# Performance work log

Hardware: AMD Instinct MI355X
Metric: run time of the kernel (lower is better)

## Reference

```python
import jax, jax.numpy as jnp
import numpy as np

SEQ, BATCH, IN = 512, 64, 1024
H, L = 512, 2


def setup_inputs() -> dict:
    key = jax.random.key(0)
    ks = jax.random.split(key, 5)
    s = 0.02
    return {
        "x": jax.random.normal(ks[0], (SEQ, BATCH, IN), dtype=jnp.float32),
        "W_ih": jax.random.normal(ks[1], (L, 2, 4 * H, IN), dtype=jnp.float32) * s,
        "b_ih": jax.random.normal(ks[2], (L, 2, 4 * H), dtype=jnp.float32) * s,
        "W_hh": jax.random.normal(ks[3], (L, 2, 4 * H, H), dtype=jnp.float32) * s,
        "b_hh": jax.random.normal(ks[4], (L, 2, 4 * H), dtype=jnp.float32) * s,
    }


def _run_direction(xs, Wi, bi, Wh, bh, hidden):
    # Precompute the input projection for all timesteps in one big GEMM.
    pre = jnp.einsum("tbd,gd->tbg", xs, Wi) + bi  # [T, B, 4H]

    def step(carry, p):
        h, c = carry
        gates = p + h @ Wh.T + bh
        i, f, g, o = jnp.split(gates, 4, axis=-1)
        # NOTE: faithful to the source module's (nonstandard) gating:
        #   c_t = c_{t-1} * sigmoid(i) + sigmoid(f) * tanh(g)
        c = c * jax.nn.sigmoid(i) + jax.nn.sigmoid(f) * jnp.tanh(g)
        h = jnp.tanh(c) * jax.nn.sigmoid(o)
        return (h, c), h

    B = xs.shape[1]
    h0 = jnp.zeros((B, hidden), xs.dtype)
    c0 = jnp.zeros((B, hidden), xs.dtype)
    _, hs = jax.lax.scan(step, (h0, c0), pre)
    return hs  # [T, B, H]


def reference(x, W_ih, b_ih, W_hh, b_hh):
    hidden = W_hh.shape[-1]
    num_layers = W_ih.shape[0]
    inp = x  # [T, B, D]
    for l in range(num_layers):
        fwd = _run_direction(inp, W_ih[l, 0], b_ih[l, 0], W_hh[l, 0], b_hh[l, 0], hidden)
        bwd = _run_direction(inp[::-1], W_ih[l, 1], b_ih[l, 1], W_hh[l, 1], b_hh[l, 1], hidden)[::-1]
        inp = jnp.concatenate([fwd, bwd], axis=-1)  # [T, B, 2H]
    return inp
```

## Files before the change

kernel.cpp:

```cpp
#include <hip/hip_runtime.h>

#define TSEQ 512
#define BATCH 64
#define DIN 1024
#define HID 512
#define G4 2048
#define CHK 64

typedef __attribute__((ext_vector_type(8))) short short8;
typedef __attribute__((ext_vector_type(4))) float floatx4;

__device__ __forceinline__ floatx4 mfma16(short8 a, short8 b, floatx4 c) {
  return __builtin_amdgcn_mfma_f32_16x16x32_bf16(a, b, c, 0, 0, 0);
}

__device__ __forceinline__ unsigned short f2bf(float f) {
  unsigned int u = __float_as_uint(f);
  unsigned int r = (u + 0x7fffu + ((u >> 16) & 1u)) >> 16;
  return (unsigned short)r;
}

__device__ __forceinline__ float sigm(float x) { return 1.f / (1.f + __expf(-x)); }
__device__ __forceinline__ float tanh_f(float x) {
  float xx = fminf(fmaxf(x, -15.f), 15.f);
  float e = __expf(2.f * xx);
  return (e - 1.f) / (e + 1.f);
}

__global__ void k_convert_x(const float* __restrict__ x, unsigned short* __restrict__ xbf, int n4) {
  int i = blockIdx.x * 256 + threadIdx.x;
  if (i >= n4) return;
  floatx4 v = reinterpret_cast<const floatx4*>(x)[i];
  union { unsigned short us[4]; unsigned long long ull; } pk;
  pk.us[0] = f2bf(v[0]); pk.us[1] = f2bf(v[1]); pk.us[2] = f2bf(v[2]); pk.us[3] = f2bf(v[3]);
  reinterpret_cast<unsigned long long*>(xbf)[i] = pk.ull;
}

__global__ void k_prep_w(const float* __restrict__ W, unsigned short* __restrict__ Wf, int K) {
  int mt = blockIdx.x, kt = blockIdx.y, ld = blockIdx.z;
  int lane = threadIdx.x;
  int rp = mt * 16 + (lane & 15);
  int row = (rp & 3) * HID + (rp >> 2);
  int k0 = kt * 32 + (lane >> 4) * 8;
  const float* src = W + (size_t)ld * G4 * K + (size_t)row * K + k0;
  unsigned short* dst = Wf + (size_t)ld * G4 * K + (((size_t)mt * (K / 32) + kt) * 64 + lane) * 8;
  for (int j = 0; j < 8; ++j) dst[j] = f2bf(src[j]);
}

__global__ void k_prep_bias(const float* __restrict__ bih, const float* __restrict__ bhh,
                            float* __restrict__ biasf) {
  int i = blockIdx.x * 256 + threadIdx.x;
  int ld = i >> 11;
  int rp = i & 2047;
  int row = (rp & 3) * HID + (rp >> 2);
  biasf[i] = bih[ld * G4 + row] + bhh[ld * G4 + row];
}

__global__ __launch_bounds__(256, 2) void k_proj(
    const unsigned short* __restrict__ xin,
    const unsigned short* __restrict__ Wf,
    const float* __restrict__ biasf,
    float* __restrict__ pre,
    int t0) {
  const int dir = blockIdx.z;
  const int w = threadIdx.x >> 6;
  const int lane = threadIdx.x & 63;
  const int quad = lane >> 4, col = lane & 15;
  const int tloc = blockIdx.y * 4 + w;
  const int tg = dir ? (TSEQ - 1 - (t0 + tloc)) : (t0 + tloc);
  const unsigned short* Wd = Wf + (size_t)dir * G4 * DIN;
  const unsigned short* xrow = xin + (size_t)tg * BATCH * DIN;

  floatx4 acc[8][4];
#pragma unroll
  for (int mi = 0; mi < 8; ++mi)
#pragma unroll
    for (int ni = 0; ni < 4; ++ni) acc[mi][ni] = (floatx4){0.f, 0.f, 0.f, 0.f};

#pragma unroll 4
  for (int kt = 0; kt < 32; ++kt) {
    short8 bfr[4];
#pragma unroll
    for (int ni = 0; ni < 4; ++ni) {
      int b = ni * 16 + col;
      bfr[ni] = *reinterpret_cast<const short8*>(xrow + (size_t)b * DIN + kt * 32 + quad * 8);
    }
#pragma unroll
    for (int mi = 0; mi < 8; ++mi) {
      size_t mt = (size_t)(blockIdx.x * 8 + mi);
      short8 afr = *reinterpret_cast<const short8*>(Wd + ((mt * 32 + kt) * 64 + lane) * 8);
#pragma unroll
      for (int ni = 0; ni < 4; ++ni) acc[mi][ni] = mfma16(afr, bfr[ni], acc[mi][ni]);
    }
  }

#pragma unroll
  for (int mi = 0; mi < 8; ++mi) {
    int gbase = blockIdx.x * 128 + mi * 16 + quad * 4;
#pragma unroll
    for (int r = 0; r < 4; ++r) {
      float bv = biasf[dir * G4 + gbase + r];
      float* prow = pre + (((size_t)dir * CHK + tloc) * G4 + gbase + r) * BATCH;
#pragma unroll
      for (int ni = 0; ni < 4; ++ni) prow[ni * 16 + col] = acc[mi][ni][r] + bv;
    }
  }
}

__global__ __launch_bounds__(256, 4) void k_step(
    const unsigned short* __restrict__ Whhf,
    const float* __restrict__ pre,
    unsigned short* act1bf,
    unsigned short* hT2,
    float* cst,
    float* __restrict__ dout,
    int s, int jloc, int layer) {
  const int dir = blockIdx.y;
  const int gb = blockIdx.x;
  const int w = threadIdx.x >> 6;
  const int lane = threadIdx.x & 63;
  const int quad = lane >> 4, col = lane & 15;
  const int b = w * 16 + col;
  const int t = dir ? (TSEQ - 1 - s) : s;

  floatx4 acc[2];
#pragma unroll
  for (int mi = 0; mi < 2; ++mi) {
#pragma unroll
    for (int r = 0; r < 4; ++r) {
      int gp = gb * 32 + mi * 16 + quad * 4 + r;
      acc[mi][r] = pre[(((size_t)dir * CHK + jloc) * G4 + gp) * BATCH + b];
    }
  }

  if (s > 0) {
    const unsigned short* hprev;
    int hstride;
    if (layer == 0) {
      int tp = dir ? t + 1 : t - 1;
      hprev = act1bf + (size_t)tp * BATCH * DIN + dir * HID;
      hstride = DIN;
    } else {
      hprev = hT2 + (size_t)(((s - 1) & 1) * 2 + dir) * BATCH * HID;
      hstride = HID;
    }
    const unsigned short* Wd = Whhf + (size_t)dir * G4 * HID;
#pragma unroll
    for (int kt = 0; kt < 16; ++kt) {
      short8 bfr = *reinterpret_cast<const short8*>(hprev + (size_t)b * hstride + kt * 32 + quad * 8);
#pragma unroll
      for (int mi = 0; mi < 2; ++mi) {
        size_t mt = (size_t)(gb * 2 + mi);
        short8 afr = *reinterpret_cast<const short8*>(Wd + ((mt * 16 + kt) * 64 + lane) * 8);
        acc[mi] = mfma16(afr, bfr, acc[mi]);
      }
    }
  }

  float* cl = cst + ((size_t)layer * 2 + dir) * HID * BATCH;
#pragma unroll
  for (int mi = 0; mi < 2; ++mi) {
    int u = gb * 8 + mi * 4 + quad;
    float si = sigm(acc[mi][0]);
    float sf = sigm(acc[mi][1]);
    float tg = tanh_f(acc[mi][2]);
    float so = sigm(acc[mi][3]);
    float cprev = (s > 0) ? cl[u * BATCH + b] : 0.f;
    float c = cprev * si + sf * tg;
    float h = tanh_f(c) * so;
    cl[u * BATCH + b] = c;
    if (layer == 0) {
      act1bf[((size_t)t * BATCH + b) * DIN + dir * HID + u] = f2bf(h);
    } else {
      hT2[((size_t)((s & 1) * 2 + dir) * BATCH + b) * HID + u] = f2bf(h);
      dout[((size_t)t * BATCH + b) * DIN + dir * HID + u] = h;
    }
  }
}

extern "C" void kernel_launch(void* const* d_in, const int* in_sizes, int n_in,
                              void* d_out, int out_size, void* d_ws, size_t ws_size,
                              hipStream_t stream) {
  const float* x = (const float*)d_in[0];
  const float* W_ih = (const float*)d_in[1];
  const float* b_ih = (const float*)d_in[2];
  const float* W_hh = (const float*)d_in[3];
  const float* b_hh = (const float*)d_in[4];
  float* dout = (float*)d_out;

  char* p = (char*)d_ws;
  auto alloc = [&](size_t bytes) {
    char* r = p;
    p += (bytes + 255) & ~(size_t)255;
    return r;
  };
  unsigned short* xbf    = (unsigned short*)alloc((size_t)TSEQ * BATCH * DIN * 2);
  unsigned short* act1bf = (unsigned short*)alloc((size_t)TSEQ * BATCH * DIN * 2);
  float*          pre    = (float*)alloc((size_t)2 * CHK * G4 * BATCH * 4);
  unsigned short* Wihf   = (unsigned short*)alloc((size_t)4 * G4 * DIN * 2);
  unsigned short* Whhf   = (unsigned short*)alloc((size_t)4 * G4 * HID * 2);
  float*          biasf  = (float*)alloc((size_t)4 * G4 * 4);
  float*          cst    = (float*)alloc((size_t)4 * HID * BATCH * 4);
  unsigned short* hT2    = (unsigned short*)alloc((size_t)4 * BATCH * HID * 2);

  size_t required = (size_t)(p - (char*)d_ws);
  if (ws_size < required) return;

  int n4 = TSEQ * BATCH * DIN / 4;
  k_convert_x<<<dim3((n4 + 255) / 256), dim3(256), 0, stream>>>(x, xbf, n4);
  k_prep_w<<<dim3(G4 / 16, DIN / 32, 4), dim3(64), 0, stream>>>(W_ih, Wihf, DIN);
  k_prep_w<<<dim3(G4 / 16, HID / 32, 4), dim3(64), 0, stream>>>(W_hh, Whhf, HID);
  k_prep_bias<<<dim3(32), dim3(256), 0, stream>>>(b_ih, b_hh, biasf);

  for (int l = 0; l < 2; ++l) {
    const unsigned short* xin = l ? act1bf : xbf;
    const unsigned short* Wfl = Wihf + (size_t)l * 2 * G4 * DIN;
    const unsigned short* Whl = Whhf + (size_t)l * 2 * G4 * HID;
    const float* bfl = biasf + (size_t)l * 2 * G4;
    for (int c = 0; c < TSEQ / CHK; ++c) {
      k_proj<<<dim3(G4 / 128, CHK / 4, 2), dim3(256), 0, stream>>>(xin, Wfl, bfl, pre, c * CHK);
      for (int j = 0; j < CHK; ++j) {
        k_step<<<dim3(G4 / 32, 2), dim3(256), 0, stream>>>(Whl, pre, act1bf, hT2, cst, dout,
                                                           c * CHK + j, j, l);
      }
    }
  }
  (void)in_sizes; (void)n_in; (void)out_size;
}
```

Measured before the change: 7.263 ms.

## Replace per-timestep launches with persistent chunk kernel and grid barrier

Instead of launching one step kernel per timestep, a single kernel now runs all 64 steps of a chunk. A per-direction atomic-counter grid barrier separates the steps. The W_hh fragments stay resident in registers across steps, the cell state is kept in registers, and the next step's preactivations are prefetched. This removes launch overhead and repeated weight and state loads, but it depends on all 128 blocks being co-resident (which holds for this grid) and adds spin-barrier latency at every step.

Result: slower. 12.14 ms (+67.1%).

```diff
diff --git a/kernel.cpp b/kernel.cpp
--- a/kernel.cpp
+++ b/kernel.cpp
@@ -54,6 +54,10 @@
   int rp = i & 2047;
   int row = (rp & 3) * HID + (rp >> 2);
   biasf[i] = bih[ld * G4 + row] + bhh[ld * G4 + row];
+}
+
+__global__ void k_zero_bar(unsigned int* bar) {
+  if (threadIdx.x < 2) bar[threadIdx.x * 64] = 0;
 }
 
 __global__ __launch_bounds__(256, 2) void k_proj(
@@ -107,75 +111,135 @@
   }
 }
 
-__global__ __launch_bounds__(256, 4) void k_step(
+__device__ __forceinline__ void dir_barrier(unsigned int* ctr, unsigned int target) {
+  __syncthreads();
+  if (threadIdx.x == 0) {
+    __threadfence();
+    __hip_atomic_fetch_add(ctr, 1u, __ATOMIC_RELAXED, __HIP_MEMORY_SCOPE_AGENT);
+    while (__hip_atomic_load(ctr, __ATOMIC_RELAXED, __HIP_MEMORY_SCOPE_AGENT) < target) {
+      __builtin_amdgcn_s_sleep(1);
+    }
+    __threadfence();
+  }
+  __syncthreads();
+}
+
+__global__ __launch_bounds__(256, 1) void k_steps(
     const unsigned short* __restrict__ Whhf,
     const float* __restrict__ pre,
     unsigned short* act1bf,
     unsigned short* hT2,
     float* cst,
     float* __restrict__ dout,
-    int s, int jloc, int layer) {
+    unsigned int* bar,
+    int t0, int layer, unsigned int bar_base) {
   const int dir = blockIdx.y;
   const int gb = blockIdx.x;
   const int w = threadIdx.x >> 6;
   const int lane = threadIdx.x & 63;
   const int quad = lane >> 4, col = lane & 15;
   const int b = w * 16 + col;
-  const int t = dir ? (TSEQ - 1 - s) : s;
-
-  floatx4 acc[2];
-#pragma unroll
-  for (int mi = 0; mi < 2; ++mi) {
+  unsigned int* ctr = bar + dir * 64;
+
+  const unsigned short* Wd = Whhf + (size_t)dir * G4 * HID;
+  short8 wfr[16][2];
+#pragma unroll
+  for (int kt = 0; kt < 16; ++kt)
+#pragma unroll
+    for (int mi = 0; mi < 2; ++mi) {
+      size_t mt = (size_t)(gb * 2 + mi);
+      wfr[kt][mi] = *reinterpret_cast<const short8*>(Wd + ((mt * 16 + kt) * 64 + lane) * 8);
+    }
+
+  float* cl = cst + ((size_t)layer * 2 + dir) * HID * BATCH;
+  const int u0 = gb * 8 + quad;
+  const int u1 = gb * 8 + 4 + quad;
+  float c0 = 0.f, c1 = 0.f;
+  if (t0 > 0) { c0 = cl[u0 * BATCH + b]; c1 = cl[u1 * BATCH + b]; }
+
+  float pf[2][4];
+#pragma unroll
+  for (int mi = 0; mi < 2; ++mi)
 #pragma unroll
     for (int r = 0; r < 4; ++r) {
       int gp = gb * 32 + mi * 16 + quad * 4 + r;
-      acc[mi][r] = pre[(((size_t)dir * CHK + jloc) * G4 + gp) * BATCH + b];
-    }
-  }
-
-  if (s > 0) {
-    const unsigned short* hprev;
-    int hstride;
+      pf[mi][r] = pre[(((size_t)dir * CHK + 0) * G4 + gp) * BATCH + b];
+    }
+
+  for (int j = 0; j < CHK; ++j) {
+    const int s = t0 + j;
+    const int t = dir ? (TSEQ - 1 - s) : s;
+
+    floatx4 acc[2];
+#pragma unroll
+    for (int mi = 0; mi < 2; ++mi)
+#pragma unroll
+      for (int r = 0; r < 4; ++r) acc[mi][r] = pf[mi][r];
+
+    if (j + 1 < CHK) {
+#pragma unroll
+      for (int mi = 0; mi < 2; ++mi)
+#pragma unroll
+        for (int r = 0; r < 4; ++r) {
+          int gp = gb * 32 + mi * 16 + quad * 4 + r;
+          pf[mi][r] = pre[(((size_t)dir * CHK + (j + 1)) * G4 + gp) * BATCH + b];
+        }
+    }
+
+    if (s > 0) {
+      const unsigned short* hprev;
+      int hstride;
+      if (layer == 0) {
+        int tp = dir ? t + 1 : t - 1;
+        hprev = act1bf + (size_t)tp * BATCH * DIN + dir * HID;
+        hstride = DIN;
+      } else {
+        hprev = hT2 + (size_t)(((s - 1) & 1) * 2 + dir) * BATCH * HID;
+        hstride = HID;
+      }
+      const unsigned short* hrow = hprev + (size_t)b * hstride;
+#pragma unroll
+      for (int kt = 0; kt < 16; ++kt) {
+        short8 bfr = *reinterpret_cast<const short8*>(hrow + kt * 32 + quad * 8);
+        acc[0] = mfma16(wfr[kt][0], bfr, acc[0]);
+        acc[1] = mfma16(wfr[kt][1], bfr, acc[1]);
+      }
+    }
+
+    float si = sigm(acc[0][0]);
+    float sf = sigm(acc[0][1]);
+    float tg = tanh_f(acc[0][2]);
+    float so = sigm(acc[0][3]);
+    c0 = c0 * si + sf * tg;
+    float h0 = tanh_f(c0) * so;
+
+    si = sigm(acc[1][0]);
+    sf = sigm(acc[1][1]);
+    tg = tanh_f(acc[1][2]);
+    so = sigm(acc[1][3]);
+    c1 = c1 * si + sf * tg;
+    float h1 = tanh_f(c1) * so;
+
     if (layer == 0) {
-      int tp = dir ? t + 1 : t - 1;
-      hprev = act1bf + (size_t)tp * BATCH * DIN + dir * HID;
-      hstride = DIN;
+      unsigned short* arow = act1bf + ((size_t)t * BATCH + b) * DIN + dir * HID;
+      arow[u0] = f2bf(h0);
+      arow[u1] = f2bf(h1);
     } else {
-      hprev = hT2 + (size_t)(((s - 1) & 1) * 2 + dir) * BATCH * HID;
-      hstride = HID;
-    }
-    const unsigned short* Wd = Whhf + (size_t)dir * G4 * HID;
-#pragma unroll
-    for (int kt = 0; kt < 16; ++kt) {
-      short8 bfr = *reinterpret_cast<const short8*>(hprev + (size_t)b * hstride + kt * 32 + quad * 8);
-#pragma unroll
-      for (int mi = 0; mi < 2; ++mi) {
-        size_t mt = (size_t)(gb * 2 + mi);
-        short8 afr = *reinterpret_cast<const short8*>(Wd + ((mt * 16 + kt) * 64 + lane) * 8);
-        acc[mi] = mfma16(afr, bfr, acc[mi]);
-      }
-    }
-  }
-
-  float* cl = cst + ((size_t)layer * 2 + dir) * HID * BATCH;
-#pragma unroll
-  for (int mi = 0; mi < 2; ++mi) {
-    int u = gb * 8 + mi * 4 + quad;
-    float si = sigm(acc[mi][0]);
-    float sf = sigm(acc[mi][1]);
-    float tg = tanh_f(acc[mi][2]);
-    float so = sigm(acc[mi][3]);
-    float cprev = (s > 0) ? cl[u * BATCH + b] : 0.f;
-    float c = cprev * si + sf * tg;
-    float h = tanh_f(c) * so;
-    cl[u * BATCH + b] = c;
-    if (layer == 0) {
-      act1bf[((size_t)t * BATCH + b) * DIN + dir * HID + u] = f2bf(h);
-    } else {
-      hT2[((size_t)((s & 1) * 2 + dir) * BATCH + b) * HID + u] = f2bf(h);
-      dout[((size_t)t * BATCH + b) * DIN + dir * HID + u] = h;
-    }
-  }
+      unsigned short* hrow2 = hT2 + ((size_t)((s & 1) * 2 + dir) * BATCH + b) * HID;
+      hrow2[u0] = f2bf(h0);
+      hrow2[u1] = f2bf(h1);
+      float* drow = dout + ((size_t)t * BATCH + b) * DIN + dir * HID;
+      drow[u0] = h0;
+      drow[u1] = h1;
+    }
+
+    if (j + 1 < CHK) {
+      dir_barrier(ctr, bar_base + (unsigned)(j + 1) * 64);
+    }
+  }
+
+  cl[u0 * BATCH + b] = c0;
+  cl[u1 * BATCH + b] = c1;
 }
 
 extern "C" void kernel_launch(void* const* d_in, const int* in_sizes, int n_in,
@@ -202,16 +266,19 @@
   float*          biasf  = (float*)alloc((size_t)4 * G4 * 4);
   float*          cst    = (float*)alloc((size_t)4 * HID * BATCH * 4);
   unsigned short* hT2    = (unsigned short*)alloc((size_t)4 * BATCH * HID * 2);
+  unsigned int*   bar    = (unsigned int*)alloc(512);
 
   size_t required = (size_t)(p - (char*)d_ws);
   if (ws_size < required) return;
 
   int n4 = TSEQ * BATCH * DIN / 4;
+  k_zero_bar<<<dim3(1), dim3(64), 0, stream>>>(bar);
   k_convert_x<<<dim3((n4 + 255) / 256), dim3(256), 0, stream>>>(x, xbf, n4);
   k_prep_w<<<dim3(G4 / 16, DIN / 32, 4), dim3(64), 0, stream>>>(W_ih, Wihf, DIN);
   k_prep_w<<<dim3(G4 / 16, HID / 32, 4), dim3(64), 0, stream>>>(W_hh, Whhf, HID);
   k_prep_bias<<<dim3(32), dim3(256), 0, stream>>>(b_ih, b_hh, biasf);
 
+  unsigned int bar_base = 0;
   for (int l = 0; l < 2; ++l) {
     const unsigned short* xin = l ? act1bf : xbf;
     const unsigned short* Wfl = Wihf + (size_t)l * 2 * G4 * DIN;
@@ -219,10 +286,9 @@
     const float* bfl = biasf + (size_t)l * 2 * G4;
     for (int c = 0; c < TSEQ / CHK; ++c) {
       k_proj<<<dim3(G4 / 128, CHK / 4, 2), dim3(256), 0, stream>>>(xin, Wfl, bfl, pre, c * CHK);
-      for (int j = 0; j < CHK; ++j) {
-        k_step<<<dim3(G4 / 32, 2), dim3(256), 0, stream>>>(Whl, pre, act1bf, hT2, cst, dout,
-                                                           c * CHK + j, j, l);
-      }
+      k_steps<<<dim3(G4 / 32, 2), dim3(256), 0, stream>>>(Whl, pre, act1bf, hT2, cst, dout,
+                                                          bar, c * CHK, l, bar_base);
+      bar_base += (unsigned)(CHK - 1) * 64;
     }
   }
   (void)in_sizes; (void)n_in; (void)out_size;
```
